# Optimization experiments

Hardware: AMD Instinct MI355X
Metric: run time of the kernel (lower is better)

The kernel has to match this reference:

```python
import jax, jax.numpy as jnp
import numpy as np

N, E, D, H = 50000, 800000, 128, 4

def setup_inputs() -> dict:
    key = jax.random.key(0)
    ks = jax.random.split(key, 6)
    x = jax.random.normal(ks[0], (N, D), dtype=jnp.float32)
    edge_index = jax.random.randint(ks[1], (2, E), 0, N, dtype=jnp.int64)
    W = jax.random.normal(ks[2], (D, H * D), dtype=jnp.float32) * (1.0 / np.sqrt(D))
    att_src = jax.random.normal(ks[3], (H, D), dtype=jnp.float32) * 0.1
    att_dst = jax.random.normal(ks[4], (H, D), dtype=jnp.float32) * 0.1
    bias = jnp.zeros((D,), dtype=jnp.float32)
    gamma = jnp.ones((D,), dtype=jnp.float32)
    beta = jnp.zeros((D,), dtype=jnp.float32)
    return {"x": x, "edge_index": edge_index, "W": W, "att_src": att_src,
            "att_dst": att_dst, "bias": bias, "gamma": gamma, "beta": beta}

def reference(x, edge_index, W, att_src, att_dst, bias, gamma, beta):
    src, dst = edge_index[0], edge_index[1]
    # GATConv: linear transform per head -> [N, H, D]
    xw = (x @ W).reshape(N, H, D)
    a_src = jnp.einsum('nhd,hd->nh', xw, att_src)  # [N, H]
    a_dst = jnp.einsum('nhd,hd->nh', xw, att_dst)  # [N, H]
    alpha = a_src[src] + a_dst[dst]                # [E, H]
    alpha = jax.nn.leaky_relu(alpha, negative_slope=0.2)
    # segment softmax over incoming edges of each dst node
    m = jax.ops.segment_max(alpha, dst, num_segments=N)   # [N, H]
    ex = jnp.exp(alpha - m[dst])                            # [E, H]
    denom = jax.ops.segment_sum(ex, dst, num_segments=N)   # [N, H]
    attn = ex / denom[dst]                                  # [E, H]
    msg = xw[src] * attn[:, :, None]                        # [E, H, D]
    agg = jax.ops.segment_sum(msg, dst, num_segments=N)    # [N, H, D]
    out = agg.mean(axis=1) + bias                           # concat=False: mean heads
    # LayerNorm (eps=1e-5)
    mu = out.mean(axis=-1, keepdims=True)
    var = out.var(axis=-1, keepdims=True)
    out = (out - mu) * jax.lax.rsqrt(var + 1e-5) * gamma + beta
    out = jax.nn.gelu(out, approximate=False)
    return out + x  # project is Identity (in_channels == out_channels)
```

## Files before the change

kernel.cpp:

```cpp
#include <hip/hip_runtime.h>
#include <hip/hip_bf16.h>
#include <hip/hip_fp16.h>
#include <math.h>

#define ND 128
#define NH 4
#define HD 512

typedef __attribute__((ext_vector_type(8))) short bf16x8;
typedef __attribute__((ext_vector_type(4))) float f32x4;

__device__ __forceinline__ unsigned pack_bf16(float a, float b) {
    unsigned ua = __float_as_uint(a), ub = __float_as_uint(b);
    ua = (ua + 0x7fffu + ((ua >> 16) & 1u)) >> 16;
    ub = (ub + 0x7fffu + ((ub >> 16) & 1u)) >> 16;
    return ua | (ub << 16);
}
__device__ __forceinline__ unsigned short bf16r(float a) {
    unsigned ua = __float_as_uint(a);
    return (unsigned short)((ua + 0x7fffu + ((ua >> 16) & 1u)) >> 16);
}
__device__ __forceinline__ float bflo(unsigned u) { return __uint_as_float(u << 16); }
__device__ __forceinline__ float bfhi(unsigned u) { return __uint_as_float(u & 0xffff0000u); }
__device__ __forceinline__ unsigned pack_half2(float a, float b) {
    __half ha = __float2half(a), hb = __float2half(b);
    return (unsigned)__half_as_ushort(ha) | ((unsigned)__half_as_ushort(hb) << 16);
}
__device__ __forceinline__ float2 h22f(unsigned u) {
    __half2 h = *(__half2*)&u;
    return __half22float2(h);
}

__global__ __launch_bounds__(256) void prep_misc(const float* __restrict__ W,
                                                 const float* __restrict__ att_src,
                                                 const float* __restrict__ att_dst,
                                                 unsigned short* __restrict__ Ws,
                                                 float* __restrict__ pt,
                                                 const int* __restrict__ dst,
                                                 int* __restrict__ cnt, int ne) {
    int b = blockIdx.x;
    if (b < 256) {
        int idx = b * 256 + threadIdx.x;
        int j = idx >> 9, K = idx & 511;
        int h = K >> 7, k = K & 127;
        Ws[idx] = bf16r(W[(size_t)k * HD + h * ND + j]);
    } else if (b == 256) {
        int k = threadIdx.x;
        if (k < ND) {
            for (int h = 0; h < NH; ++h) {
                float ps = 0.f, pd = 0.f;
                for (int d = 0; d < ND; ++d) {
                    float wv = W[(size_t)k * HD + h * ND + d];
                    ps = fmaf(wv, att_src[h * ND + d], ps);
                    pd = fmaf(wv, att_dst[h * ND + d], pd);
                }
                pt[h * ND + k] = ps;
                pt[(4 + h) * ND + k] = pd;
            }
        }
    } else {
        int e = (b - 257) * 256 + threadIdx.x;
        if (e < ne) atomicAdd(&cnt[dst[e]], 1);
    }
}

__global__ __launch_bounds__(256) void k_a_xb(const float* __restrict__ x,
                                              const float* __restrict__ pt,
                                              unsigned* __restrict__ xb,
                                              float* __restrict__ a_src,
                                              float* __restrict__ a_dst, int n) {
    __shared__ float pl[8 * ND];
    { int t = threadIdx.x; ((float4*)pl)[t] = ((const float4*)pt)[t]; }
    __syncthreads();
    int wave = (blockIdx.x * 256 + threadIdx.x) >> 6;
    int lane = threadIdx.x & 63;
    if (wave >= n) return;
    float2 xv = ((const float2*)(x + (size_t)wave * ND))[lane];
    xb[(size_t)wave * 64 + lane] = pack_bf16(xv.x, xv.y);
#pragma unroll
    for (int o = 0; o < 8; ++o) {
        float2 pv = ((const float2*)(pl + o * ND))[lane];
        float v = xv.x * pv.x + xv.y * pv.y;
#pragma unroll
        for (int off = 1; off < 64; off <<= 1) v += __shfl_xor(v, off);
        if (lane == 0) {
            if (o < 4) a_src[(size_t)wave * NH + o] = v;
            else       a_dst[(size_t)wave * NH + (o - 4)] = v;
        }
    }
}

__global__ __launch_bounds__(256) void scanA(const int* __restrict__ cnt,
                                             int* __restrict__ partial,
                                             int* __restrict__ bsum, int n) {
    __shared__ int sh[256];
    int gid = blockIdx.x * 256 + threadIdx.x;
    int v = (gid < n) ? cnt[gid] : 0;
    int val = v;
    sh[threadIdx.x] = val;
    __syncthreads();
#pragma unroll
    for (int off = 1; off < 256; off <<= 1) {
        int add = (threadIdx.x >= off) ? sh[threadIdx.x - off] : 0;
        __syncthreads();
        val += add;
        sh[threadIdx.x] = val;
        __syncthreads();
    }
    if (gid < n) partial[gid] = val - v;
    if (threadIdx.x == 255) bsum[blockIdx.x] = val;
}

__global__ __launch_bounds__(256) void scanBC(const int* __restrict__ partial,
                                              const int* __restrict__ bsum,
                                              int* __restrict__ starts,
                                              int* __restrict__ cursor,
                                              int n, int ne, int nb) {
    __shared__ int sh[256];
    int t = threadIdx.x;
    int v = (t < nb) ? bsum[t] : 0;
    int val = v;
    sh[t] = val;
    __syncthreads();
#pragma unroll
    for (int off = 1; off < 256; off <<= 1) {
        int add = (t >= off) ? sh[t - off] : 0;
        __syncthreads();
        val += add;
        sh[t] = val;
        __syncthreads();
    }
    int myoff = (blockIdx.x == 0) ? 0 : sh[blockIdx.x - 1];
    int gid = blockIdx.x * 256 + t;
    if (gid < n) {
        int s = partial[gid] + myoff;
        starts[gid] = s;
        cursor[gid] = s;
    }
    if (gid == 0) starts[n] = ne;
}

__global__ __launch_bounds__(256) void scatter_edges_w(const int* __restrict__ src,
                                                       const int* __restrict__ dst,
                                                       const float* __restrict__ a_src,
                                                       const float* __restrict__ a_dst,
                                                       int* __restrict__ cursor,
                                                       uint4* __restrict__ eperm, int ne) {
    int e = blockIdx.x * 256 + threadIdx.x;
    if (e < ne) {
        int s = src[e], t = dst[e];
        float4 as = *(const float4*)(a_src + (size_t)s * NH);
        float4 ad = *(const float4*)(a_dst + (size_t)t * NH);
        float A0 = as.x + ad.x, A1 = as.y + ad.y, A2 = as.z + ad.z, A3 = as.w + ad.w;
        A0 = (A0 > 0.f) ? A0 : 0.2f * A0;
        A1 = (A1 > 0.f) ? A1 : 0.2f * A1;
        A2 = (A2 > 0.f) ? A2 : 0.2f * A2;
        A3 = (A3 > 0.f) ? A3 : 0.2f * A3;
        float e0 = expf(A0), e1 = expf(A1), e2 = expf(A2), e3 = expf(A3);
        int pos = atomicAdd(&cursor[t], 1);
        uint4 ev;
        ev.x = (unsigned)s;
        ev.y = pack_half2(e0, e1);
        ev.z = pack_half2(e2, e3);
        ev.w = 0u;
        eperm[pos] = ev;
    }
}

#define FMA16()                                                            \
    { float f0 = bflo(xv.x), f1 = bfhi(xv.x), f2 = bflo(xv.y), f3 = bfhi(xv.y); \
      acc[0] = fmaf(w01.x, f0, acc[0]);  acc[1] = fmaf(w01.x, f1, acc[1]);  \
      acc[2] = fmaf(w01.x, f2, acc[2]);  acc[3] = fmaf(w01.x, f3, acc[3]);  \
      acc[4] = fmaf(w01.y, f0, acc[4]);  acc[5] = fmaf(w01.y, f1, acc[5]);  \
      acc[6] = fmaf(w01.y, f2, acc[6]);  acc[7] = fmaf(w01.y, f3, acc[7]);  \
      acc[8] = fmaf(w23.x, f0, acc[8]);  acc[9] = fmaf(w23.x, f1, acc[9]);  \
      acc[10] = fmaf(w23.x, f2, acc[10]); acc[11] = fmaf(w23.x, f3, acc[11]); \
      acc[12] = fmaf(w23.y, f0, acc[12]); acc[13] = fmaf(w23.y, f1, acc[13]); \
      acc[14] = fmaf(w23.y, f2, acc[14]); acc[15] = fmaf(w23.y, f3, acc[15]); }

__global__ __launch_bounds__(256) void node_agg(const uint4* __restrict__ eperm,
                                                const int* __restrict__ starts,
                                                const uint2* __restrict__ xb2,
                                                unsigned* __restrict__ u, int n) {
    int node = (blockIdx.x * 256 + threadIdx.x) >> 6;
    int lane = threadIdx.x & 63;
    if (node >= n) return;
    const int slot = lane & 31;
    const int half = lane >> 5;

    int s0 = starts[node], s1 = starts[node + 1];

    float den0 = 0.f, den1 = 0.f, den2 = 0.f, den3 = 0.f;
    float acc[16];
#pragma unroll
    for (int j = 0; j < 16; ++j) acc[j] = 0.f;

    for (int base = s0; base < s1; base += 16) {
        int rem = s1 - base; if (rem > 16) rem = 16;
        uint4 ev = {0u, 0u, 0u, 0u};
        if (lane < rem) ev = eperm[base + lane];
        {
            float2 dl = h22f(ev.y), dh = h22f(ev.z);
            den0 += dl.x; den1 += dl.y; den2 += dh.x; den3 += dh.y;
        }
        if (rem == 16) {
#pragma unroll
            for (int pp = 0; pp < 8; ++pp) {
                int j2 = 2 * pp + half;
                int s = __shfl((int)ev.x, j2);
                unsigned uy = __shfl(ev.y, j2);
                unsigned uz = __shfl(ev.z, j2);
                uint2 xv = xb2[(size_t)s * 32 + slot];
                float2 w01 = h22f(uy), w23 = h22f(uz);
                FMA16();
            }
        } else {
            for (int jj = 0; jj < rem; jj += 2) {
                int j2 = jj + half;
                bool valid = (j2 < rem);
                int j2c = valid ? j2 : jj;
                int s = __shfl((int)ev.x, j2c);
                unsigned uy = __shfl(ev.y, j2c);
                unsigned uz = __shfl(ev.z, j2c);
                uint2 xv = xb2[(size_t)s * 32 + slot];
                float2 w01 = h22f(uy), w23 = h22f(uz);
                float m = valid ? 1.f : 0.f;
                w01.x *= m; w01.y *= m; w23.x *= m; w23.y *= m;
                FMA16();
            }
        }
    }

#pragma unroll
    for (int off = 1; off < 64; off <<= 1) {
        den0 += __shfl_xor(den0, off);
        den1 += __shfl_xor(den1, off);
        den2 += __shfl_xor(den2, off);
        den3 += __shfl_xor(den3, off);
    }
    float i0 = (den0 > 0.f) ? 0.25f / den0 : 0.f;
    float i1 = (den1 > 0.f) ? 0.25f / den1 : 0.f;
    float i2 = (den2 > 0.f) ? 0.25f / den2 : 0.f;
    float i3 = (den3 > 0.f) ? 0.25f / den3 : 0.f;

    float v[16];
#pragma unroll
    for (int f = 0; f < 4; ++f) {
        v[0 + f]  = acc[0 + f]  * i0;
        v[4 + f]  = acc[4 + f]  * i1;
        v[8 + f]  = acc[8 + f]  * i2;
        v[12 + f] = acc[12 + f] * i3;
    }
#pragma unroll
    for (int j = 0; j < 16; ++j) v[j] += __shfl_xor(v[j], 32);

#pragma unroll
    for (int hh = 0; hh < 2; ++hh) {
        int h = half * 2 + hh;
        uint2 val;
        val.x = pack_bf16(v[h * 4 + 0], v[h * 4 + 1]);
        val.y = pack_bf16(v[h * 4 + 2], v[h * 4 + 3]);
        ((uint2*)u)[(size_t)node * 128 + h * 32 + slot] = val;
    }
}

__global__ __launch_bounds__(256, 2) void gemm_out(
        const unsigned short* __restrict__ u, const unsigned short* __restrict__ Ws,
        const float* __restrict__ x, const float* __restrict__ bias,
        const float* __restrict__ gamma, const float* __restrict__ beta,
        float* __restrict__ out, int n) {
    __shared__ char lds[65536];
    char* As = lds;
    char* Bs = lds + 32768;
    const int t = threadIdx.x;
    const int row0 = blockIdx.x * 128;
    const int l = t & 63, w = t >> 6;
    const int eid = l & 15, g = l >> 4;

    f32x4 acc[2][8];
#pragma unroll
    for (int mt = 0; mt < 2; ++mt)
#pragma unroll
        for (int nr = 0; nr < 8; ++nr) acc[mt][nr] = (f32x4){0.f, 0.f, 0.f, 0.f};

    for (int kc = 0; kc < 4; ++kc) {
        __syncthreads();
#pragma unroll
        for (int i = 0; i < 8; ++i) {
            int c = t + i * 256;
            int m = c >> 4, kb = c & 15;
            int row = row0 + m;
            uint4 pv = {0u, 0u, 0u, 0u};
            if (row < n) pv = *(const uint4*)(u + (size_t)row * HD + kc * 128 + kb * 8);
            *(uint4*)(As + m * 256 + ((kb * 16) ^ ((m & 7) << 4))) = pv;
        }
#pragma unroll
        for (int i = 0; i < 8; ++i) {
            int c = t + i * 256;
            int nl = c >> 4, kb = c & 15;
            uint4 pv = *(const uint4*)(Ws + (size_t)nl * HD + kc * 128 + kb * 8);
            *(uint4*)(Bs + nl * 256 + ((kb * 16) ^ ((nl & 7) << 4))) = pv;
        }
        __syncthreads();

        const int swz = (eid & 7) << 4;
#pragma unroll
        for (int ks = 0; ks < 4; ++ks) {
            int koff = (ks * 64 + g * 16) ^ swz;
            bf16x8 a0 = *(const bf16x8*)(As + (w * 32 + eid) * 256 + koff);
            bf16x8 a1 = *(const bf16x8*)(As + (w * 32 + 16 + eid) * 256 + koff);
#pragma unroll
            for (int nr = 0; nr < 8; ++nr) {
                bf16x8 b = *(const bf16x8*)(Bs + (nr * 16 + eid) * 256 + koff);
                acc[0][nr] = __builtin_amdgcn_mfma_f32_16x16x32_bf16(a0, b, acc[0][nr], 0, 0, 0);
                acc[1][nr] = __builtin_amdgcn_mfma_f32_16x16x32_bf16(a1, b, acc[1][nr], 0, 0, 0);
            }
        }
    }

    __syncthreads();
    float* T = (float*)lds;
#pragma unroll
    for (int mt = 0; mt < 2; ++mt)
#pragma unroll
        for (int ri = 0; ri < 4; ++ri) {
            int rl = w * 32 + mt * 16 + g * 4 + ri;
#pragma unroll
            for (int nr = 0; nr < 8; ++nr)
                T[rl * 128 + nr * 16 + eid] = acc[mt][nr][ri];
        }
    __syncthreads();

    float2 bv = ((const float2*)bias)[l];
    float2 gv = ((const float2*)gamma)[l];
    float2 tb = ((const float2*)beta)[l];
    for (int i = 0; i < 32; ++i) {
        int row = w * 32 + i;
        int grow = row0 + row;
        if (grow >= n) break;
        float2 c2 = ((float2*)(T + row * 128))[l];
        c2.x += bv.x; c2.y += bv.y;
        float s = c2.x + c2.y, s2 = c2.x * c2.x + c2.y * c2.y;
#pragma unroll
        for (int off = 1; off < 64; off <<= 1) {
            s += __shfl_xor(s, off);
            s2 += __shfl_xor(s2, off);
        }
        float mu = s * (1.0f / ND);
        float var = s2 * (1.0f / ND) - mu * mu;
        var = fmaxf(var, 0.0f);
        float inv = rsqrtf(var + 1e-5f);
        float2 xres = ((const float2*)(x + (size_t)grow * ND))[l];
        float y0 = (c2.x - mu) * inv * gv.x + tb.x;
        float y1 = (c2.y - mu) * inv * gv.y + tb.y;
        y0 = 0.5f * y0 * (1.0f + erff(y0 * 0.70710678118654752f)) + xres.x;
        y1 = 0.5f * y1 * (1.0f + erff(y1 * 0.70710678118654752f)) + xres.y;
        float2 ov = {y0, y1};
        ((float2*)(out + (size_t)grow * ND))[l] = ov;
    }
}

extern "C" void kernel_launch(void* const* d_in, const int* in_sizes, int n_in,
                              void* d_out, int out_size, void* d_ws, size_t ws_size,
                              hipStream_t stream) {
    const float* x       = (const float*)d_in[0];
    const int*   edge    = (const int*)d_in[1];
    const float* W       = (const float*)d_in[2];
    const float* att_src = (const float*)d_in[3];
    const float* att_dst = (const float*)d_in[4];
    const float* bias    = (const float*)d_in[5];
    const float* gamma   = (const float*)d_in[6];
    const float* beta    = (const float*)d_in[7];
    float* out = (float*)d_out;

    const int n  = in_sizes[0] / ND;
    const int ne = in_sizes[1] / 2;
    const int* src = edge;
    const int* dst = edge + ne;

    const int nb = (n + 255) / 256;

    char* wsp = (char*)d_ws;
    unsigned* xb        = (unsigned*)wsp;        wsp += (size_t)n * 64 * sizeof(unsigned);
    unsigned short* u   = (unsigned short*)wsp;  wsp += (size_t)n * HD * sizeof(short);
    unsigned short* Ws  = (unsigned short*)wsp;  wsp += (size_t)ND * HD * sizeof(short);
    float* pt      = (float*)wsp;               wsp += (size_t)8 * ND * sizeof(float);
    float* a_src   = (float*)wsp;               wsp += (size_t)n * NH * sizeof(float);
    float* a_dst   = (float*)wsp;               wsp += (size_t)n * NH * sizeof(float);
    uint4* eperm   = (uint4*)wsp;               wsp += (size_t)ne * sizeof(uint4);
    int*   cnt     = (int*)wsp;                 wsp += (size_t)n * sizeof(int);
    int*   partial = (int*)wsp;                 wsp += (size_t)n * sizeof(int);
    int*   bsum    = (int*)wsp;                 wsp += 256 * sizeof(int);
    int*   starts  = (int*)wsp;                 wsp += (size_t)(n + 1) * sizeof(int);
    int*   cursor  = (int*)wsp;                 wsp += (size_t)n * sizeof(int);

    (void)hipMemsetAsync(cnt, 0, (size_t)n * sizeof(int), stream);

    prep_misc<<<257 + (ne + 255) / 256, 256, 0, stream>>>(W, att_src, att_dst,
                                                          Ws, pt, dst, cnt, ne);
    k_a_xb<<<(n + 3) / 4, 256, 0, stream>>>(x, pt, xb, a_src, a_dst, n);

    scanA<<<nb, 256, 0, stream>>>(cnt, partial, bsum, n);
    scanBC<<<nb, 256, 0, stream>>>(partial, bsum, starts, cursor, n, ne, nb);
    scatter_edges_w<<<(ne + 255) / 256, 256, 0, stream>>>(src, dst, a_src, a_dst,
                                                          cursor, eperm, ne);

    node_agg<<<(n + 3) / 4, 256, 0, stream>>>(eperm, starts, (const uint2*)xb,
                                              (unsigned*)u, n);

    gemm_out<<<(n + 127) / 128, 256, 0, stream>>>(u, Ws, x, bias, gamma, beta, out, n);
}
```

Baseline: 246.5 us.

## Use packed FMA and direct edge loads in aggregation; shrink output GEMM tile

```diff
diff --git a/kernel.cpp b/kernel.cpp
--- a/kernel.cpp
+++ b/kernel.cpp
@@ -9,6 +9,7 @@
 
 typedef __attribute__((ext_vector_type(8))) short bf16x8;
 typedef __attribute__((ext_vector_type(4))) float f32x4;
+typedef __attribute__((ext_vector_type(2))) float f32x2;
 
 __device__ __forceinline__ unsigned pack_bf16(float a, float b) {
     unsigned ua = __float_as_uint(a), ub = __float_as_uint(b);
@@ -167,16 +168,13 @@
     }
 }
 
-#define FMA16()                                                            \
-    { float f0 = bflo(xv.x), f1 = bfhi(xv.x), f2 = bflo(xv.y), f3 = bfhi(xv.y); \
-      acc[0] = fmaf(w01.x, f0, acc[0]);  acc[1] = fmaf(w01.x, f1, acc[1]);  \
-      acc[2] = fmaf(w01.x, f2, acc[2]);  acc[3] = fmaf(w01.x, f3, acc[3]);  \
-      acc[4] = fmaf(w01.y, f0, acc[4]);  acc[5] = fmaf(w01.y, f1, acc[5]);  \
-      acc[6] = fmaf(w01.y, f2, acc[6]);  acc[7] = fmaf(w01.y, f3, acc[7]);  \
-      acc[8] = fmaf(w23.x, f0, acc[8]);  acc[9] = fmaf(w23.x, f1, acc[9]);  \
-      acc[10] = fmaf(w23.x, f2, acc[10]); acc[11] = fmaf(w23.x, f3, acc[11]); \
-      acc[12] = fmaf(w23.y, f0, acc[12]); acc[13] = fmaf(w23.y, f1, acc[13]); \
-      acc[14] = fmaf(w23.y, f2, acc[14]); acc[15] = fmaf(w23.y, f3, acc[15]); }
+#define PKFMA8()                                                           \
+    { f32x2 xlo = {bflo(xv.x), bfhi(xv.x)};                                \
+      f32x2 xhi = {bflo(xv.y), bfhi(xv.y)};                                \
+      acc2[0] += xlo * w01.x; acc2[1] += xhi * w01.x;                      \
+      acc2[2] += xlo * w01.y; acc2[3] += xhi * w01.y;                      \
+      acc2[4] += xlo * w23.x; acc2[5] += xhi * w23.x;                      \
+      acc2[6] += xlo * w23.y; acc2[7] += xhi * w23.y; }
 
 __global__ __launch_bounds__(256) void node_agg(const uint4* __restrict__ eperm,
                                                 const int* __restrict__ starts,
@@ -191,42 +189,36 @@
     int s0 = starts[node], s1 = starts[node + 1];
 
     float den0 = 0.f, den1 = 0.f, den2 = 0.f, den3 = 0.f;
-    float acc[16];
-#pragma unroll
-    for (int j = 0; j < 16; ++j) acc[j] = 0.f;
+    f32x2 acc2[8];
+#pragma unroll
+    for (int j = 0; j < 8; ++j) acc2[j] = (f32x2){0.f, 0.f};
 
     for (int base = s0; base < s1; base += 16) {
         int rem = s1 - base; if (rem > 16) rem = 16;
-        uint4 ev = {0u, 0u, 0u, 0u};
-        if (lane < rem) ev = eperm[base + lane];
         {
+            uint4 ev = {0u, 0u, 0u, 0u};
+            if (lane < rem) ev = eperm[base + lane];
             float2 dl = h22f(ev.y), dh = h22f(ev.z);
             den0 += dl.x; den1 += dl.y; den2 += dh.x; den3 += dh.y;
         }
         if (rem == 16) {
 #pragma unroll
             for (int pp = 0; pp < 8; ++pp) {
-                int j2 = 2 * pp + half;
-                int s = __shfl((int)ev.x, j2);
-                unsigned uy = __shfl(ev.y, j2);
-                unsigned uz = __shfl(ev.z, j2);
-                uint2 xv = xb2[(size_t)s * 32 + slot];
-                float2 w01 = h22f(uy), w23 = h22f(uz);
-                FMA16();
+                uint4 ev2 = eperm[base + 2 * pp + half];
+                uint2 xv = xb2[((unsigned)ev2.x << 5) + slot];
+                float2 w01 = h22f(ev2.y), w23 = h22f(ev2.z);
+                PKFMA8();
             }
         } else {
             for (int jj = 0; jj < rem; jj += 2) {
                 int j2 = jj + half;
                 bool valid = (j2 < rem);
-                int j2c = valid ? j2 : jj;
-                int s = __shfl((int)ev.x, j2c);
-                unsigned uy = __shfl(ev.y, j2c);
-                unsigned uz = __shfl(ev.z, j2c);
-                uint2 xv = xb2[(size_t)s * 32 + slot];
-                float2 w01 = h22f(uy), w23 = h22f(uz);
+                uint4 ev2 = eperm[base + (valid ? j2 : jj)];
+                uint2 xv = xb2[((unsigned)ev2.x << 5) + slot];
+                float2 w01 = h22f(ev2.y), w23 = h22f(ev2.z);
                 float m = valid ? 1.f : 0.f;
                 w01.x *= m; w01.y *= m; w23.x *= m; w23.y *= m;
-                FMA16();
+                PKFMA8();
             }
         }
     }
@@ -245,11 +237,12 @@
 
     float v[16];
 #pragma unroll
-    for (int f = 0; f < 4; ++f) {
-        v[0 + f]  = acc[0 + f]  * i0;
-        v[4 + f]  = acc[4 + f]  * i1;
-        v[8 + f]  = acc[8 + f]  * i2;
-        v[12 + f] = acc[12 + f] * i3;
+    for (int hh4 = 0; hh4 < 4; ++hh4) {
+        float ih = (hh4 == 0) ? i0 : (hh4 == 1) ? i1 : (hh4 == 2) ? i2 : i3;
+        v[hh4 * 4 + 0] = acc2[hh4 * 2].x * ih;
+        v[hh4 * 4 + 1] = acc2[hh4 * 2].y * ih;
+        v[hh4 * 4 + 2] = acc2[hh4 * 2 + 1].x * ih;
+        v[hh4 * 4 + 3] = acc2[hh4 * 2 + 1].y * ih;
     }
 #pragma unroll
     for (int j = 0; j < 16; ++j) v[j] += __shfl_xor(v[j], 32);
@@ -264,29 +257,27 @@
     }
 }
 
-__global__ __launch_bounds__(256, 2) void gemm_out(
+__global__ __launch_bounds__(256, 3) void gemm_out(
         const unsigned short* __restrict__ u, const unsigned short* __restrict__ Ws,
         const float* __restrict__ x, const float* __restrict__ bias,
         const float* __restrict__ gamma, const float* __restrict__ beta,
         float* __restrict__ out, int n) {
-    __shared__ char lds[65536];
+    __shared__ char lds[49152];
     char* As = lds;
-    char* Bs = lds + 32768;
+    char* Bs = lds + 16384;
     const int t = threadIdx.x;
-    const int row0 = blockIdx.x * 128;
+    const int row0 = blockIdx.x * 64;
     const int l = t & 63, w = t >> 6;
     const int eid = l & 15, g = l >> 4;
 
-    f32x4 acc[2][8];
-#pragma unroll
-    for (int mt = 0; mt < 2; ++mt)
-#pragma unroll
-        for (int nr = 0; nr < 8; ++nr) acc[mt][nr] = (f32x4){0.f, 0.f, 0.f, 0.f};
+    f32x4 acc[8];
+#pragma unroll
+    for (int nr = 0; nr < 8; ++nr) acc[nr] = (f32x4){0.f, 0.f, 0.f, 0.f};
 
     for (int kc = 0; kc < 4; ++kc) {
         __syncthreads();
 #pragma unroll
-        for (int i = 0; i < 8; ++i) {
+        for (int i = 0; i < 4; ++i) {
             int c = t + i * 256;
             int m = c >> 4, kb = c & 15;
             int row = row0 + m;
@@ -307,13 +298,11 @@
 #pragma unroll
         for (int ks = 0; ks < 4; ++ks) {
             int koff = (ks * 64 + g * 16) ^ swz;
-            bf16x8 a0 = *(const bf16x8*)(As + (w * 32 + eid) * 256 + koff);
-            bf16x8 a1 = *(const bf16x8*)(As + (w * 32 + 16 + eid) * 256 + koff);
+            bf16x8 a0 = *(const bf16x8*)(As + (w * 16 + eid) * 256 + koff);
 #pragma unroll
             for (int nr = 0; nr < 8; ++nr) {
                 bf16x8 b = *(const bf16x8*)(Bs + (nr * 16 + eid) * 256 + koff);
-                acc[0][nr] = __builtin_amdgcn_mfma_f32_16x16x32_bf16(a0, b, acc[0][nr], 0, 0, 0);
-                acc[1][nr] = __builtin_amdgcn_mfma_f32_16x16x32_bf16(a1, b, acc[1][nr], 0, 0, 0);
+                acc[nr] = __builtin_amdgcn_mfma_f32_16x16x32_bf16(a0, b, acc[nr], 0, 0, 0);
             }
         }
     }
@@ -321,21 +310,19 @@
     __syncthreads();
     float* T = (float*)lds;
 #pragma unroll
-    for (int mt = 0; mt < 2; ++mt)
-#pragma unroll
-        for (int ri = 0; ri < 4; ++ri) {
-            int rl = w * 32 + mt * 16 + g * 4 + ri;
-#pragma unroll
-            for (int nr = 0; nr < 8; ++nr)
-                T[rl * 128 + nr * 16 + eid] = acc[mt][nr][ri];
-        }
+    for (int ri = 0; ri < 4; ++ri) {
+        int rl = w * 16 + g * 4 + ri;
+#pragma unroll
+        for (int nr = 0; nr < 8; ++nr)
+            T[rl * 128 + nr * 16 + eid] = acc[nr][ri];
+    }
     __syncthreads();
 
     float2 bv = ((const float2*)bias)[l];
     float2 gv = ((const float2*)gamma)[l];
     float2 tb = ((const float2*)beta)[l];
-    for (int i = 0; i < 32; ++i) {
-        int row = w * 32 + i;
+    for (int i = 0; i < 16; ++i) {
+        int row = w * 16 + i;
         int grow = row0 + row;
         if (grow >= n) break;
         float2 c2 = ((float2*)(T + row * 128))[l];
@@ -408,5 +395,5 @@
     node_agg<<<(n + 3) / 4, 256, 0, stream>>>(eperm, starts, (const uint2*)xb,
                                               (unsigned*)u, n);
 
-    gemm_out<<<(n + 127) / 128, 256, 0, stream>>>(u, Ws, x, bias, gamma, beta, out, n);
-}
+    gemm_out<<<(n + 63) / 64, 256, 0, stream>>>(u, Ws, x, bias, gamma, beta, out, n);
+}
```

Measured after the change: 253.1 us. 1.03x slower.

## Fuse node aggregation with output GEMM and LayerNorm; merge attention-score and scan kernels

Applied to the files above, without the earlier changes.

```diff
diff --git a/kernel.cpp b/kernel.cpp
--- a/kernel.cpp
+++ b/kernel.cpp
@@ -64,51 +64,54 @@
     }
 }
 
-__global__ __launch_bounds__(256) void k_a_xb(const float* __restrict__ x,
-                                              const float* __restrict__ pt,
-                                              unsigned* __restrict__ xb,
-                                              float* __restrict__ a_src,
-                                              float* __restrict__ a_dst, int n) {
+__global__ __launch_bounds__(256) void ka_scanA(const float* __restrict__ x,
+                                                const float* __restrict__ pt,
+                                                unsigned* __restrict__ xb,
+                                                float* __restrict__ a_src,
+                                                float* __restrict__ a_dst,
+                                                const int* __restrict__ cnt,
+                                                int* __restrict__ partial,
+                                                int* __restrict__ bsum,
+                                                int n, int nbA) {
     __shared__ float pl[8 * ND];
-    { int t = threadIdx.x; ((float4*)pl)[t] = ((const float4*)pt)[t]; }
-    __syncthreads();
-    int wave = (blockIdx.x * 256 + threadIdx.x) >> 6;
-    int lane = threadIdx.x & 63;
-    if (wave >= n) return;
-    float2 xv = ((const float2*)(x + (size_t)wave * ND))[lane];
-    xb[(size_t)wave * 64 + lane] = pack_bf16(xv.x, xv.y);
-#pragma unroll
-    for (int o = 0; o < 8; ++o) {
-        float2 pv = ((const float2*)(pl + o * ND))[lane];
-        float v = xv.x * pv.x + xv.y * pv.y;
-#pragma unroll
-        for (int off = 1; off < 64; off <<= 1) v += __shfl_xor(v, off);
-        if (lane == 0) {
-            if (o < 4) a_src[(size_t)wave * NH + o] = v;
-            else       a_dst[(size_t)wave * NH + (o - 4)] = v;
-        }
-    }
-}
-
-__global__ __launch_bounds__(256) void scanA(const int* __restrict__ cnt,
-                                             int* __restrict__ partial,
-                                             int* __restrict__ bsum, int n) {
     __shared__ int sh[256];
-    int gid = blockIdx.x * 256 + threadIdx.x;
-    int v = (gid < n) ? cnt[gid] : 0;
-    int val = v;
-    sh[threadIdx.x] = val;
-    __syncthreads();
-#pragma unroll
-    for (int off = 1; off < 256; off <<= 1) {
-        int add = (threadIdx.x >= off) ? sh[threadIdx.x - off] : 0;
+    if ((int)blockIdx.x < nbA) {
+        { int t = threadIdx.x; ((float4*)pl)[t] = ((const float4*)pt)[t]; }
         __syncthreads();
-        val += add;
+        int wave = (blockIdx.x * 256 + threadIdx.x) >> 6;
+        int lane = threadIdx.x & 63;
+        if (wave >= n) return;
+        float2 xv = ((const float2*)(x + (size_t)wave * ND))[lane];
+        xb[(size_t)wave * 64 + lane] = pack_bf16(xv.x, xv.y);
+#pragma unroll
+        for (int o = 0; o < 8; ++o) {
+            float2 pv = ((const float2*)(pl + o * ND))[lane];
+            float v = xv.x * pv.x + xv.y * pv.y;
+#pragma unroll
+            for (int off = 1; off < 64; off <<= 1) v += __shfl_xor(v, off);
+            if (lane == 0) {
+                if (o < 4) a_src[(size_t)wave * NH + o] = v;
+                else       a_dst[(size_t)wave * NH + (o - 4)] = v;
+            }
+        }
+    } else {
+        int bid = blockIdx.x - nbA;
+        int gid = bid * 256 + threadIdx.x;
+        int v = (gid < n) ? cnt[gid] : 0;
+        int val = v;
         sh[threadIdx.x] = val;
         __syncthreads();
-    }
-    if (gid < n) partial[gid] = val - v;
-    if (threadIdx.x == 255) bsum[blockIdx.x] = val;
+#pragma unroll
+        for (int off = 1; off < 256; off <<= 1) {
+            int add = (threadIdx.x >= off) ? sh[threadIdx.x - off] : 0;
+            __syncthreads();
+            val += add;
+            sh[threadIdx.x] = val;
+            __syncthreads();
+        }
+        if (gid < n) partial[gid] = val - v;
+        if (threadIdx.x == 255) bsum[bid] = val;
+    }
 }
 
 __global__ __launch_bounds__(256) void scanBC(const int* __restrict__ partial,
@@ -178,169 +181,139 @@
       acc[12] = fmaf(w23.y, f0, acc[12]); acc[13] = fmaf(w23.y, f1, acc[13]); \
       acc[14] = fmaf(w23.y, f2, acc[14]); acc[15] = fmaf(w23.y, f3, acc[15]); }
 
-__global__ __launch_bounds__(256) void node_agg(const uint4* __restrict__ eperm,
-                                                const int* __restrict__ starts,
-                                                const uint2* __restrict__ xb2,
-                                                unsigned* __restrict__ u, int n) {
-    int node = (blockIdx.x * 256 + threadIdx.x) >> 6;
-    int lane = threadIdx.x & 63;
-    if (node >= n) return;
-    const int slot = lane & 31;
-    const int half = lane >> 5;
-
-    int s0 = starts[node], s1 = starts[node + 1];
-
-    float den0 = 0.f, den1 = 0.f, den2 = 0.f, den3 = 0.f;
-    float acc[16];
-#pragma unroll
-    for (int j = 0; j < 16; ++j) acc[j] = 0.f;
-
-    for (int base = s0; base < s1; base += 16) {
-        int rem = s1 - base; if (rem > 16) rem = 16;
-        uint4 ev = {0u, 0u, 0u, 0u};
-        if (lane < rem) ev = eperm[base + lane];
-        {
-            float2 dl = h22f(ev.y), dh = h22f(ev.z);
-            den0 += dl.x; den1 += dl.y; den2 += dh.x; den3 += dh.y;
-        }
-        if (rem == 16) {
-#pragma unroll
-            for (int pp = 0; pp < 8; ++pp) {
-                int j2 = 2 * pp + half;
-                int s = __shfl((int)ev.x, j2);
-                unsigned uy = __shfl(ev.y, j2);
-                unsigned uz = __shfl(ev.z, j2);
-                uint2 xv = xb2[(size_t)s * 32 + slot];
-                float2 w01 = h22f(uy), w23 = h22f(uz);
-                FMA16();
-            }
-        } else {
-            for (int jj = 0; jj < rem; jj += 2) {
-                int j2 = jj + half;
-                bool valid = (j2 < rem);
-                int j2c = valid ? j2 : jj;
-                int s = __shfl((int)ev.x, j2c);
-                unsigned uy = __shfl(ev.y, j2c);
-                unsigned uz = __shfl(ev.z, j2c);
-                uint2 xv = xb2[(size_t)s * 32 + slot];
-                float2 w01 = h22f(uy), w23 = h22f(uz);
-                float m = valid ? 1.f : 0.f;
-                w01.x *= m; w01.y *= m; w23.x *= m; w23.y *= m;
-                FMA16();
-            }
-        }
-    }
-
-#pragma unroll
-    for (int off = 1; off < 64; off <<= 1) {
-        den0 += __shfl_xor(den0, off);
-        den1 += __shfl_xor(den1, off);
-        den2 += __shfl_xor(den2, off);
-        den3 += __shfl_xor(den3, off);
-    }
-    float i0 = (den0 > 0.f) ? 0.25f / den0 : 0.f;
-    float i1 = (den1 > 0.f) ? 0.25f / den1 : 0.f;
-    float i2 = (den2 > 0.f) ? 0.25f / den2 : 0.f;
-    float i3 = (den3 > 0.f) ? 0.25f / den3 : 0.f;
-
-    float v[16];
-#pragma unroll
-    for (int f = 0; f < 4; ++f) {
-        v[0 + f]  = acc[0 + f]  * i0;
-        v[4 + f]  = acc[4 + f]  * i1;
-        v[8 + f]  = acc[8 + f]  * i2;
-        v[12 + f] = acc[12 + f] * i3;
-    }
-#pragma unroll
-    for (int j = 0; j < 16; ++j) v[j] += __shfl_xor(v[j], 32);
-
-#pragma unroll
-    for (int hh = 0; hh < 2; ++hh) {
-        int h = half * 2 + hh;
-        uint2 val;
-        val.x = pack_bf16(v[h * 4 + 0], v[h * 4 + 1]);
-        val.y = pack_bf16(v[h * 4 + 2], v[h * 4 + 3]);
-        ((uint2*)u)[(size_t)node * 128 + h * 32 + slot] = val;
-    }
-}
-
-__global__ __launch_bounds__(256, 2) void gemm_out(
-        const unsigned short* __restrict__ u, const unsigned short* __restrict__ Ws,
+__global__ __launch_bounds__(256) void node_agg_fused(
+        const uint4* __restrict__ eperm, const int* __restrict__ starts,
+        const uint2* __restrict__ xb2, const unsigned short* __restrict__ Ws,
         const float* __restrict__ x, const float* __restrict__ bias,
         const float* __restrict__ gamma, const float* __restrict__ beta,
         float* __restrict__ out, int n) {
-    __shared__ char lds[65536];
-    char* As = lds;
-    char* Bs = lds + 32768;
-    const int t = threadIdx.x;
-    const int row0 = blockIdx.x * 128;
-    const int l = t & 63, w = t >> 6;
-    const int eid = l & 15, g = l >> 4;
-
-    f32x4 acc[2][8];
-#pragma unroll
-    for (int mt = 0; mt < 2; ++mt)
-#pragma unroll
-        for (int nr = 0; nr < 8; ++nr) acc[mt][nr] = (f32x4){0.f, 0.f, 0.f, 0.f};
-
-    for (int kc = 0; kc < 4; ++kc) {
-        __syncthreads();
-#pragma unroll
-        for (int i = 0; i < 8; ++i) {
-            int c = t + i * 256;
-            int m = c >> 4, kb = c & 15;
-            int row = row0 + m;
-            uint4 pv = {0u, 0u, 0u, 0u};
-            if (row < n) pv = *(const uint4*)(u + (size_t)row * HD + kc * 128 + kb * 8);
-            *(uint4*)(As + m * 256 + ((kb * 16) ^ ((m & 7) << 4))) = pv;
-        }
-#pragma unroll
-        for (int i = 0; i < 8; ++i) {
-            int c = t + i * 256;
-            int nl = c >> 4, kb = c & 15;
-            uint4 pv = *(const uint4*)(Ws + (size_t)nl * HD + kc * 128 + kb * 8);
-            *(uint4*)(Bs + nl * 256 + ((kb * 16) ^ ((nl & 7) << 4))) = pv;
-        }
-        __syncthreads();
-
-        const int swz = (eid & 7) << 4;
-#pragma unroll
-        for (int ks = 0; ks < 4; ++ks) {
-            int koff = (ks * 64 + g * 16) ^ swz;
-            bf16x8 a0 = *(const bf16x8*)(As + (w * 32 + eid) * 256 + koff);
-            bf16x8 a1 = *(const bf16x8*)(As + (w * 32 + 16 + eid) * 256 + koff);
-#pragma unroll
-            for (int nr = 0; nr < 8; ++nr) {
-                bf16x8 b = *(const bf16x8*)(Bs + (nr * 16 + eid) * 256 + koff);
-                acc[0][nr] = __builtin_amdgcn_mfma_f32_16x16x32_bf16(a0, b, acc[0][nr], 0, 0, 0);
-                acc[1][nr] = __builtin_amdgcn_mfma_f32_16x16x32_bf16(a1, b, acc[1][nr], 0, 0, 0);
+    __shared__ char lds[16384];
+
+    const int w = threadIdx.x >> 6;
+    const int lane = threadIdx.x & 63;
+    const int slot = lane & 31;
+    const int half = lane >> 5;
+    const int node0 = blockIdx.x * 16;
+
+    for (int i = 0; i < 4; ++i) {
+        const int nl = w * 4 + i;
+        const int node = node0 + nl;
+        int s0 = 0, s1 = 0;
+        if (node < n) { s0 = starts[node]; s1 = starts[node + 1]; }
+
+        float den0 = 0.f, den1 = 0.f, den2 = 0.f, den3 = 0.f;
+        float acc[16];
+#pragma unroll
+        for (int j = 0; j < 16; ++j) acc[j] = 0.f;
+
+        for (int base = s0; base < s1; base += 16) {
+            int rem = s1 - base; if (rem > 16) rem = 16;
+            uint4 ev = {0u, 0u, 0u, 0u};
+            if (lane < rem) ev = eperm[base + lane];
+            {
+                float2 dl = h22f(ev.y), dh = h22f(ev.z);
+                den0 += dl.x; den1 += dl.y; den2 += dh.x; den3 += dh.y;
             }
-        }
-    }
-
+            if (rem == 16) {
+#pragma unroll
+                for (int pp = 0; pp < 8; ++pp) {
+                    int j2 = 2 * pp + half;
+                    int s = __shfl((int)ev.x, j2);
+                    unsigned uy = __shfl(ev.y, j2);
+                    unsigned uz = __shfl(ev.z, j2);
+                    uint2 xv = xb2[(size_t)s * 32 + slot];
+                    float2 w01 = h22f(uy), w23 = h22f(uz);
+                    FMA16();
+                }
+            } else {
+                for (int jj = 0; jj < rem; jj += 2) {
+                    int j2 = jj + half;
+                    bool valid = (j2 < rem);
+                    int j2c = valid ? j2 : jj;
+                    int s = __shfl((int)ev.x, j2c);
+                    unsigned uy = __shfl(ev.y, j2c);
+                    unsigned uz = __shfl(ev.z, j2c);
+                    uint2 xv = xb2[(size_t)s * 32 + slot];
+                    float2 w01 = h22f(uy), w23 = h22f(uz);
+                    float m = valid ? 1.f : 0.f;
+                    w01.x *= m; w01.y *= m; w23.x *= m; w23.y *= m;
+                    FMA16();
+                }
+            }
+        }
+
+#pragma unroll
+        for (int off = 1; off < 64; off <<= 1) {
+            den0 += __shfl_xor(den0, off);
+            den1 += __shfl_xor(den1, off);
+            den2 += __shfl_xor(den2, off);
+            den3 += __shfl_xor(den3, off);
+        }
+        float i0 = (den0 > 0.f) ? 0.25f / den0 : 0.f;
+        float i1 = (den1 > 0.f) ? 0.25f / den1 : 0.f;
+        float i2 = (den2 > 0.f) ? 0.25f / den2 : 0.f;
+        float i3 = (den3 > 0.f) ? 0.25f / den3 : 0.f;
+
+        float v[16];
+#pragma unroll
+        for (int f = 0; f < 4; ++f) {
+            v[0 + f]  = acc[0 + f]  * i0;
+            v[4 + f]  = acc[4 + f]  * i1;
+            v[8 + f]  = acc[8 + f]  * i2;
+            v[12 + f] = acc[12 + f] * i3;
+        }
+#pragma unroll
+        for (int j = 0; j < 16; ++j) v[j] += __shfl_xor(v[j], 32);
+
+#pragma unroll
+        for (int hh = 0; hh < 2; ++hh) {
+            int h = half * 2 + hh;
+            int Kb = (h * ND + slot * 4) * 2;
+            int boff = nl * 1024 + ((Kb & ~15) ^ ((nl & 7) << 4)) + (Kb & 8);
+            uint2 val;
+            val.x = pack_bf16(v[h * 4 + 0], v[h * 4 + 1]);
+            val.y = pack_bf16(v[h * 4 + 2], v[h * 4 + 3]);
+            *(uint2*)(lds + boff) = val;
+        }
+    }
     __syncthreads();
-    float* T = (float*)lds;
-#pragma unroll
-    for (int mt = 0; mt < 2; ++mt)
-#pragma unroll
-        for (int ri = 0; ri < 4; ++ri) {
-            int rl = w * 32 + mt * 16 + g * 4 + ri;
-#pragma unroll
-            for (int nr = 0; nr < 8; ++nr)
-                T[rl * 128 + nr * 16 + eid] = acc[mt][nr][ri];
-        }
+
+    const int g16 = lane >> 4;
+    const int e16 = lane & 15;
+    f32x4 cacc[2];
+    cacc[0] = (f32x4){0.f, 0.f, 0.f, 0.f};
+    cacc[1] = (f32x4){0.f, 0.f, 0.f, 0.f};
+#pragma unroll
+    for (int t = 0; t < 16; ++t) {
+        int K0 = t * 32 + 8 * g16;
+        bf16x8 a = *(const bf16x8*)(lds + e16 * 1024 + ((K0 * 2) ^ ((e16 & 7) << 4)));
+#pragma unroll
+        for (int c2 = 0; c2 < 2; ++c2) {
+            int c = w * 2 + c2;
+            bf16x8 b = *(const bf16x8*)(Ws + (size_t)(c * 16 + e16) * HD + K0);
+            cacc[c2] = __builtin_amdgcn_mfma_f32_16x16x32_bf16(a, b, cacc[c2], 0, 0, 0);
+        }
+    }
     __syncthreads();
 
-    float2 bv = ((const float2*)bias)[l];
-    float2 gv = ((const float2*)gamma)[l];
-    float2 tb = ((const float2*)beta)[l];
-    for (int i = 0; i < 32; ++i) {
-        int row = w * 32 + i;
-        int grow = row0 + row;
+    float* C = (float*)lds;
+#pragma unroll
+    for (int c2 = 0; c2 < 2; ++c2)
+#pragma unroll
+        for (int ri = 0; ri < 4; ++ri)
+            C[(g16 * 4 + ri) * 128 + (w * 2 + c2) * 16 + e16] = cacc[c2][ri];
+    __syncthreads();
+
+    float2 bv = ((const float2*)bias)[lane];
+    float2 gv = ((const float2*)gamma)[lane];
+    float2 tb = ((const float2*)beta)[lane];
+    for (int i = 0; i < 4; ++i) {
+        int row = w * 4 + i;
+        int grow = node0 + row;
         if (grow >= n) break;
-        float2 c2 = ((float2*)(T + row * 128))[l];
-        c2.x += bv.x; c2.y += bv.y;
-        float s = c2.x + c2.y, s2 = c2.x * c2.x + c2.y * c2.y;
+        float2 c2v = ((float2*)(C + row * 128))[lane];
+        c2v.x += bv.x; c2v.y += bv.y;
+        float s = c2v.x + c2v.y, s2 = c2v.x * c2v.x + c2v.y * c2v.y;
 #pragma unroll
         for (int off = 1; off < 64; off <<= 1) {
             s += __shfl_xor(s, off);
@@ -350,13 +323,13 @@
         float var = s2 * (1.0f / ND) - mu * mu;
         var = fmaxf(var, 0.0f);
         float inv = rsqrtf(var + 1e-5f);
-        float2 xres = ((const float2*)(x + (size_t)grow * ND))[l];
-        float y0 = (c2.x - mu) * inv * gv.x + tb.x;
-        float y1 = (c2.y - mu) * inv * gv.y + tb.y;
+        float2 xres = ((const float2*)(x + (size_t)grow * ND))[lane];
+        float y0 = (c2v.x - mu) * inv * gv.x + tb.x;
+        float y1 = (c2v.y - mu) * inv * gv.y + tb.y;
         y0 = 0.5f * y0 * (1.0f + erff(y0 * 0.70710678118654752f)) + xres.x;
         y1 = 0.5f * y1 * (1.0f + erff(y1 * 0.70710678118654752f)) + xres.y;
         float2 ov = {y0, y1};
-        ((float2*)(out + (size_t)grow * ND))[l] = ov;
+        ((float2*)(out + (size_t)grow * ND))[lane] = ov;
     }
 }
 
@@ -378,11 +351,11 @@
     const int* src = edge;
     const int* dst = edge + ne;
 
-    const int nb = (n + 255) / 256;
+    const int nb  = (n + 255) / 256;
+    const int nbA = (n + 3) / 4;
 
     char* wsp = (char*)d_ws;
     unsigned* xb        = (unsigned*)wsp;        wsp += (size_t)n * 64 * sizeof(unsigned);
-    unsigned short* u   = (unsigned short*)wsp;  wsp += (size_t)n * HD * sizeof(short);
     unsigned short* Ws  = (unsigned short*)wsp;  wsp += (size_t)ND * HD * sizeof(short);
     float* pt      = (float*)wsp;               wsp += (size_t)8 * ND * sizeof(float);
     float* a_src   = (float*)wsp;               wsp += (size_t)n * NH * sizeof(float);
@@ -398,15 +371,15 @@
 
     prep_misc<<<257 + (ne + 255) / 256, 256, 0, stream>>>(W, att_src, att_dst,
                                                           Ws, pt, dst, cnt, ne);
-    k_a_xb<<<(n + 3) / 4, 256, 0, stream>>>(x, pt, xb, a_src, a_dst, n);
-
-    scanA<<<nb, 256, 0, stream>>>(cnt, partial, bsum, n);
+
+    ka_scanA<<<nbA + nb, 256, 0, stream>>>(x, pt, xb, a_src, a_dst,
+                                           cnt, partial, bsum, n, nbA);
+
     scanBC<<<nb, 256, 0, stream>>>(partial, bsum, starts, cursor, n, ne, nb);
+
     scatter_edges_w<<<(ne + 255) / 256, 256, 0, stream>>>(src, dst, a_src, a_dst,
                                                           cursor, eperm, ne);
 
-    node_agg<<<(n + 3) / 4, 256, 0, stream>>>(eperm, starts, (const uint2*)xb,
-                                              (unsigned*)u, n);
-
-    gemm_out<<<(n + 127) / 128, 256, 0, stream>>>(u, Ws, x, bias, gamma, beta, out, n);
-}
+    node_agg_fused<<<(n + 15) / 16, 256, 0, stream>>>(eperm, starts, (const uint2*)xb,
+                                                      Ws, x, bias, gamma, beta, out, n);
+}
```

Measured after the change: 256.2 us. +3.9%, slower.
